# Performance work log

Hardware: AMD Instinct MI355X
Metric: run time of the kernel (lower is better)

Reference implementation:

```python
import jax, jax.numpy as jnp
import numpy as np

IN_CHANNELS = 64
NY, NX = 496, 432
N_VOXELS = 64000
BATCH = 4


def setup_inputs() -> dict:
    key = jax.random.key(0)
    k1, k2, k3, k4 = jax.random.split(key, 4)
    voxel_features = jax.random.normal(k1, (N_VOXELS, IN_CHANNELS), dtype=jnp.float32)
    b = jax.random.randint(k2, (N_VOXELS,), 0, BATCH, dtype=jnp.int32)
    y = jax.random.randint(k3, (N_VOXELS,), 0, NY, dtype=jnp.int32)
    x = jax.random.randint(k4, (N_VOXELS,), 0, NX, dtype=jnp.int32)
    z = jnp.zeros((N_VOXELS,), dtype=jnp.int32)
    coors = jnp.stack([b, z, y, x], axis=1)  # (N, 4): [batch, z, y, x]
    return {"voxel_features": voxel_features, "coors": coors, "batch_size": BATCH}


def reference(voxel_features, coors, batch_size):
    # Fused scatter: flat index into (batch * ny * nx) canvas, single .at[].set.
    # Original overwrites on duplicate coords; pillar coords are unique by construction.
    C = voxel_features.shape[1]
    flat_idx = (coors[:, 0].astype(jnp.int32) * (NY * NX)
                + coors[:, 2].astype(jnp.int32) * NX
                + coors[:, 3].astype(jnp.int32))  # (N,)
    canvas = jnp.zeros((batch_size * NY * NX, C), dtype=voxel_features.dtype)
    canvas = canvas.at[flat_idx].set(voxel_features)
    # (B*ny*nx, C) -> (B, C, ny, nx)
    canvas = canvas.reshape(batch_size, NY, NX, C).transpose(0, 3, 1, 2)
    return canvas
```

## Files before the change

kernel.cpp:

```cpp
#include <hip/hip_runtime.h>


#define C_CH 64
#define NY_ 496
#define NX_ 432
#define NPIX (NY_ * NX_)
#define NVOX 64000
#define BATCH_ 4
#define PIX4 (NPIX / 4)

__global__ void pps_winners(const int* __restrict__ coors, int* __restrict__ ws, int n) {
    int i = blockIdx.x * blockDim.x + threadIdx.x;
    if (i >= n) return;
    const int4 cv = reinterpret_cast<const int4*>(coors)[i];
    int flat = cv.x * NPIX + cv.z * NX_ + cv.w;
    atomicMax(&ws[flat], i);
}

__global__ void pps_gather(const float* __restrict__ vf,
                           const int* __restrict__ ws,
                           float* __restrict__ out) {
    long tid = (long)blockIdx.x * blockDim.x + threadIdx.x;
    int bc = (int)(tid / PIX4);
    int p4 = (int)(tid - (long)bc * PIX4);
    int b = bc >> 6;
    int c = bc & 63;
    int pix = p4 * 4;

    const int4 w = *reinterpret_cast<const int4*>(&ws[b * NPIX + pix]);
    float4 o;
    o.x = (w.x >= 0) ? vf[(long)w.x * C_CH + c] : 0.0f;
    o.y = (w.y >= 0) ? vf[(long)w.y * C_CH + c] : 0.0f;
    o.z = (w.z >= 0) ? vf[(long)w.z * C_CH + c] : 0.0f;
    o.w = (w.w >= 0) ? vf[(long)w.w * C_CH + c] : 0.0f;
    *reinterpret_cast<float4*>(&out[(long)bc * NPIX + pix]) = o;
}

extern "C" void kernel_launch(void* const* d_in, const int* in_sizes, int n_in,
                              void* d_out, int out_size, void* d_ws, size_t ws_size,
                              hipStream_t stream) {
    const float* vf = (const float*)d_in[0];
    const int* coors = (const int*)d_in[1];
    float* out = (float*)d_out;
    int* ws = (int*)d_ws;

    hipMemsetAsync(ws, 0xFF, (size_t)BATCH_ * NPIX * sizeof(int), stream);

    {
        int threads = 256;
        int blocks = (NVOX + threads - 1) / threads;
        pps_winners<<<blocks, threads, 0, stream>>>(coors, ws, NVOX);
    }

    {
        long total = (long)BATCH_ * C_CH * PIX4;
        int threads = 256;
        long blocks = (total + threads - 1) / threads;
        pps_gather<<<(int)blocks, threads, 0, stream>>>(vf, ws, out);
    }
}
```

Baseline: 248.5 us.

## Transpose voxel features to channel-major and widen gather with nontemporal stores

A new prep kernel merges the winner atomicMax pass with a shared-memory transpose of voxel features into a channel-major buffer in workspace. The gather then reads each channel's values from one contiguous 256 KB row instead of striding across 256-byte voxel rows. This is meant to improve cache locality of the random reads. Each thread now produces 8 pixels and writes them with nontemporal stores, which cuts index math and keeps the large output from polluting the cache. The cost is an extra 16 MB write and read for the transposed copy, and the workspace must be large enough to hold it.

```diff
diff --git a/kernel.cpp b/kernel.cpp
--- a/kernel.cpp
+++ b/kernel.cpp
@@ -7,33 +7,79 @@
 #define NPIX (NY_ * NX_)
 #define NVOX 64000
 #define BATCH_ 4
-#define PIX4 (NPIX / 4)
+#define PIX8 (NPIX / 8)
 
-__global__ void pps_winners(const int* __restrict__ coors, int* __restrict__ ws, int n) {
-    int i = blockIdx.x * blockDim.x + threadIdx.x;
-    if (i >= n) return;
-    const int4 cv = reinterpret_cast<const int4*>(coors)[i];
-    int flat = cv.x * NPIX + cv.z * NX_ + cv.w;
-    atomicMax(&ws[flat], i);
+typedef float f32x4 __attribute__((ext_vector_type(4)));
+
+__global__ void pps_prep(const float* __restrict__ vf,
+                         const int* __restrict__ coors,
+                         int* __restrict__ ws,
+                         float* __restrict__ vfT) {
+    __shared__ float tile[64][65];
+
+    int gid = blockIdx.x * 256 + threadIdx.x;
+    if (gid < NVOX) {
+        const int4 cv = reinterpret_cast<const int4*>(coors)[gid];
+        atomicMax(&ws[cv.x * NPIX + cv.z * NX_ + cv.w], gid);
+    }
+
+    int n0 = blockIdx.x * 64;
+    int tr = threadIdx.x >> 2;
+    int tc = (threadIdx.x & 3) * 16;
+
+    const float4* src = reinterpret_cast<const float4*>(vf + (long)(n0 + tr) * C_CH + tc);
+    #pragma unroll
+    for (int j = 0; j < 4; ++j) {
+        float4 v = src[j];
+        tile[tr][tc + j * 4 + 0] = v.x;
+        tile[tr][tc + j * 4 + 1] = v.y;
+        tile[tr][tc + j * 4 + 2] = v.z;
+        tile[tr][tc + j * 4 + 3] = v.w;
+    }
+    __syncthreads();
+
+    int c = threadIdx.x >> 2;
+    int ns = (threadIdx.x & 3) * 16;
+    float* dst = vfT + (long)c * NVOX + n0 + ns;
+    #pragma unroll
+    for (int j = 0; j < 4; ++j) {
+        float4 v;
+        v.x = tile[ns + j * 4 + 0][c];
+        v.y = tile[ns + j * 4 + 1][c];
+        v.z = tile[ns + j * 4 + 2][c];
+        v.w = tile[ns + j * 4 + 3][c];
+        reinterpret_cast<float4*>(dst)[j] = v;
+    }
 }
 
-__global__ void pps_gather(const float* __restrict__ vf,
+__global__ void pps_gather(const float* __restrict__ vfT,
                            const int* __restrict__ ws,
                            float* __restrict__ out) {
-    long tid = (long)blockIdx.x * blockDim.x + threadIdx.x;
-    int bc = (int)(tid / PIX4);
-    int p4 = (int)(tid - (long)bc * PIX4);
+    int tid = blockIdx.x * blockDim.x + threadIdx.x;
+    int bc = tid / PIX8;
+    int p8 = tid - bc * PIX8;
     int b = bc >> 6;
     int c = bc & 63;
-    int pix = p4 * 4;
+    int pix = p8 * 8;
 
-    const int4 w = *reinterpret_cast<const int4*>(&ws[b * NPIX + pix]);
-    float4 o;
-    o.x = (w.x >= 0) ? vf[(long)w.x * C_CH + c] : 0.0f;
-    o.y = (w.y >= 0) ? vf[(long)w.y * C_CH + c] : 0.0f;
-    o.z = (w.z >= 0) ? vf[(long)w.z * C_CH + c] : 0.0f;
-    o.w = (w.w >= 0) ? vf[(long)w.w * C_CH + c] : 0.0f;
-    *reinterpret_cast<float4*>(&out[(long)bc * NPIX + pix]) = o;
+    const int4* wp = reinterpret_cast<const int4*>(&ws[b * NPIX + pix]);
+    const int4 w0 = wp[0];
+    const int4 w1 = wp[1];
+    const float* __restrict__ row = vfT + (long)c * NVOX;
+
+    f32x4 o0, o1;
+    o0.x = (w0.x >= 0) ? row[w0.x] : 0.0f;
+    o0.y = (w0.y >= 0) ? row[w0.y] : 0.0f;
+    o0.z = (w0.z >= 0) ? row[w0.z] : 0.0f;
+    o0.w = (w0.w >= 0) ? row[w0.w] : 0.0f;
+    o1.x = (w1.x >= 0) ? row[w1.x] : 0.0f;
+    o1.y = (w1.y >= 0) ? row[w1.y] : 0.0f;
+    o1.z = (w1.z >= 0) ? row[w1.z] : 0.0f;
+    o1.w = (w1.w >= 0) ? row[w1.w] : 0.0f;
+
+    f32x4* op = reinterpret_cast<f32x4*>(&out[(long)bc * NPIX + pix]);
+    __builtin_nontemporal_store(o0, op);
+    __builtin_nontemporal_store(o1, op + 1);
 }
 
 extern "C" void kernel_launch(void* const* d_in, const int* in_sizes, int n_in,
@@ -43,19 +89,14 @@
     const int* coors = (const int*)d_in[1];
     float* out = (float*)d_out;
     int* ws = (int*)d_ws;
+    float* vfT = (float*)(ws + (size_t)BATCH_ * NPIX);
 
-    hipMemsetAsync(ws, 0xFF, (size_t)BATCH_ * NPIX * sizeof(int), stream);
+    (void)hipMemsetAsync(ws, 0xFF, (size_t)BATCH_ * NPIX * sizeof(int), stream);
+
+    pps_prep<<<NVOX / 64, 256, 0, stream>>>(vf, coors, ws, vfT);
 
     {
-        int threads = 256;
-        int blocks = (NVOX + threads - 1) / threads;
-        pps_winners<<<blocks, threads, 0, stream>>>(coors, ws, NVOX);
-    }
-
-    {
-        long total = (long)BATCH_ * C_CH * PIX4;
-        int threads = 256;
-        long blocks = (total + threads - 1) / threads;
-        pps_gather<<<(int)blocks, threads, 0, stream>>>(vf, ws, out);
+        int total = BATCH_ * C_CH * PIX8;
+        pps_gather<<<total / 256, 256, 0, stream>>>(vfT, ws, out);
     }
 }
```

Measured after the change: 354.9 us. 42.8% more time.
